# Kernel optimization log

Hardware: AMD Instinct MI355X
Metric: run time of the kernel (lower is better)

The kernel has to match this reference:

```python
import jax, jax.numpy as jnp
import numpy as np

B, IN_DIM, D, C = 4096, 1024, 128, 10000
H, HD = 4, 32  # heads, head_dim (D = H*HD)
EXP = 4        # ffn expansion
LN_EPS = 1e-5


def _ln(x, g, b):
    m = x.mean(-1, keepdims=True)
    v = ((x - m) ** 2).mean(-1, keepdims=True)
    return (x - m) / jnp.sqrt(v + LN_EPS) * g + b


def setup_inputs() -> dict:
    key = jax.random.key(0)
    ks = jax.random.split(key, 16)
    s = 0.02
    return {
        "x": jax.random.normal(ks[0], (B, IN_DIM), jnp.float32),
        # projector
        "W1": jax.random.normal(ks[1], (IN_DIM, 2 * D), jnp.float32) * s,
        "b1": jnp.zeros((2 * D,), jnp.float32),
        "W2": jax.random.normal(ks[2], (2 * D, D), jnp.float32) * s,
        "b2": jnp.zeros((D,), jnp.float32),
        # fractal block: MHA
        "in_w": jax.random.normal(ks[3], (D, 3 * D), jnp.float32) * s,
        "in_b": jnp.zeros((3 * D,), jnp.float32),
        "out_w": jax.random.normal(ks[4], (D, D), jnp.float32) * s,
        "out_b": jnp.zeros((D,), jnp.float32),
        # fractal block: FFN
        "fw1": jax.random.normal(ks[5], (D, EXP * D), jnp.float32) * s,
        "fb1": jnp.zeros((EXP * D,), jnp.float32),
        "fw2": jax.random.normal(ks[6], (EXP * D, D), jnp.float32) * s,
        "fb2": jnp.zeros((D,), jnp.float32),
        # layernorms
        "g1": jnp.ones((D,), jnp.float32), "bt1": jnp.zeros((D,), jnp.float32),
        "g2": jnp.ones((D,), jnp.float32), "bt2": jnp.zeros((D,), jnp.float32),
        # curvature, prototypes, euclidean head
        "log_c": jnp.array(0.0, jnp.float32),  # log(1.0)
        "prototypes": jax.random.normal(ks[7], (C, D), jnp.float32) * 0.1,
        "euc_w": jax.random.normal(ks[8], (D, C), jnp.float32) * s,
        "euc_b": jnp.zeros((C,), jnp.float32),
    }


def reference(x, W1, b1, W2, b2, in_w, in_b, out_w, out_b,
              fw1, fb1, fw2, fb2, g1, bt1, g2, bt2,
              log_c, prototypes, euc_w, euc_b):
    # ---- projector MLP (exact GELU, as torch default) ----
    t = jax.nn.gelu(x @ W1 + b1, approximate=False) @ W2 + b2  # (B, D)

    # ---- FractalBlock on seq_len=1 ----
    xs = t[:, None, :]  # (B, 1, D)
    qkv = xs @ in_w + in_b  # (B, 1, 3D)
    q, k, v = jnp.split(qkv, 3, axis=-1)
    q = q.reshape(B, 1, H, HD)
    k = k.reshape(B, 1, H, HD)
    v = v.reshape(B, 1, H, HD)
    scores = jnp.einsum("bqhd,bkhd->bhqk", q, k) / jnp.sqrt(jnp.float32(HD))
    w = jax.nn.softmax(scores, axis=-1)  # seq=1 -> all ones
    attn = jnp.einsum("bhqk,bkhd->bqhd", w, v).reshape(B, 1, D)
    attn = attn @ out_w + out_b
    xs = _ln(xs + attn, g1, bt1)
    ffn = jax.nn.gelu(xs @ fw1 + fb1, approximate=False) @ fw2 + fb2
    xs = _ln(xs + ffn, g2, bt2)
    t = xs[:, 0, :]  # (B, D) tangent

    # ---- curvature ----
    c = jnp.clip(jnp.exp(log_c), 1e-4, 10.0)
    c = jnp.maximum(jnp.abs(c), 1e-6)
    sqrt_c = jnp.sqrt(c)

    # ---- exp map to Poincare ball ----
    v_norm = jnp.maximum(jnp.linalg.norm(t, axis=-1, keepdims=True), 1e-10)
    emb = jnp.tanh(sqrt_c * v_norm / 2) * t / (sqrt_c * v_norm)
    e_norm = jnp.linalg.norm(emb, axis=-1, keepdims=True)
    max_norm = (1 - 1e-5) / sqrt_c
    emb = emb * jnp.minimum(max_norm / jnp.maximum(e_norm, 1e-6), 1.0)  # (B, D)

    # ---- project prototypes inside ball ----
    p_norm = jnp.linalg.norm(prototypes, axis=-1, keepdims=True)
    protos = prototypes * jnp.minimum(max_norm / jnp.maximum(p_norm, 1e-6), 1.0)  # (C, D)

    e2 = jnp.sum(emb * emb, axis=-1)      # (B,)
    p2 = jnp.sum(protos * protos, axis=-1)  # (C,)
    diff_sq = jnp.maximum(e2[:, None] + p2[None, :] - 2.0 * emb @ protos.T, 1e-10)  # (B, C)
    denom = (1 - c * jnp.minimum(e2, 1 - 1e-5))[:, None] * (1 - c * jnp.minimum(p2, 1 - 1e-5))[None, :]
    arg = 1 + 2 * diff_sq / jnp.maximum(denom, 1e-6)
    dists = 2 / sqrt_c * jnp.arccosh(jnp.maximum(arg, 1.0 + 1e-6))  # (B, C)

    hyp_logits = -dists
    euc_logits = t @ euc_w + euc_b
    return hyp_logits, euc_logits, emb
```

## Files before the change

### kernel.cpp

```cpp
#include <hip/hip_runtime.h>
#include <cmath>


using bf16x8 = __attribute__((ext_vector_type(8))) __bf16;
using f32x4  = __attribute__((ext_vector_type(4))) float;

#define DEVINL __device__ __forceinline__

DEVINL unsigned short f2b(float f) {
    unsigned int u = __builtin_bit_cast(unsigned int, f);
    u = (u + 0x7fffu + ((u >> 16) & 1u)) >> 16;
    return (unsigned short)u;
}

DEVINL float gelu_exact(float x) {
    return 0.5f * x * (1.0f + erff(x * 0.70710678118654752440f));
}

DEVINL float get_c(const float* logc) {
    float c = expf(logc[0]);
    c = fminf(fmaxf(c, 1e-4f), 10.0f);
    return fmaxf(fabsf(c), 1e-6f);
}

DEVINL void async16(const unsigned short* g, unsigned short* l) {
    __builtin_amdgcn_global_load_lds(
        (const __attribute__((address_space(1))) void*)g,
        (__attribute__((address_space(3))) void*)l, 16, 0, 0);
}


DEVINL void t_cvt(const float* __restrict__ src, unsigned short* __restrict__ dst,
                  int K, int N, int Npad, int ld, int off, int tblk, int tid,
                  float tile[32][33]) {
    int kbCount = K >> 5;
    int kb = (tblk % kbCount) * 32, nb = (tblk / kbCount) * 32;
    int tx = tid & 31, ty = tid >> 5;
    #pragma unroll
    for (int i = 0; i < 32; i += 8) {
        int k = kb + ty + i, n = nb + tx;
        tile[ty + i][tx] = (k < K && n < N) ? src[(size_t)k * ld + off + n] : 0.0f;
    }
    __syncthreads();
    #pragma unroll
    for (int i = 0; i < 32; i += 8) {
        int n = nb + ty + i, k = kb + tx;
        if (n < Npad && k < K) dst[(size_t)n * K + k] = f2b(tile[tx][ty + i]);
    }
}

#define PB0 4096
#define PB1 (PB0 + 256)
#define PB2 (PB1 + 64)
#define PB3 (PB2 + 64)
#define PB4 (PB3 + 1264)
#define PB5 (PB4 + 2528)

__global__ void k_prep(const float* __restrict__ x, const float* __restrict__ W1,
                       const float* __restrict__ fw1, const float* __restrict__ fw2,
                       const float* __restrict__ euc_w, const float* __restrict__ P,
                       const float* __restrict__ logc,
                       unsigned short* __restrict__ xbf, unsigned short* __restrict__ W1T,
                       unsigned short* __restrict__ FW1T, unsigned short* __restrict__ FW2T,
                       unsigned short* __restrict__ EUCWT, unsigned short* __restrict__ PROTB,
                       float* __restrict__ p2a, float* __restrict__ dpa) {
    __shared__ float tile[32][33];
    int b = blockIdx.x, tid = threadIdx.x;
    if (b < PB0) {
        int i = b * 256 + tid;
        float4 v = ((const float4*)x)[i];
        ushort4 o;
        o.x = f2b(v.x); o.y = f2b(v.y); o.z = f2b(v.z); o.w = f2b(v.w);
        ((ushort4*)xbf)[i] = o;
    } else if (b < PB1) {
        t_cvt(W1, W1T, 1024, 256, 256, 256, 0, b - PB0, tid, tile);
    } else if (b < PB2) {
        t_cvt(fw1, FW1T, 128, 512, 512, 512, 0, b - PB1, tid, tile);
    } else if (b < PB3) {
        t_cvt(fw2, FW2T, 512, 128, 128, 128, 0, b - PB2, tid, tile);
    } else if (b < PB4) {
        t_cvt(euc_w, EUCWT, 128, 10000, 10112, 10000, 0, b - PB3, tid, tile);
    } else {
        int lane = tid & 63;
        int row = (b - PB4) * 4 + (tid >> 6);
        size_t base = (size_t)row * 128;
        if (row < 10000) {
            float a = P[base + lane], bb = P[base + 64 + lane];
            float n2 = a * a + bb * bb;
            #pragma unroll
            for (int m = 32; m > 0; m >>= 1) n2 += __shfl_xor(n2, m, 64);
            float c = get_c(logc);
            float sq = sqrtf(c);
            float mx = (1.0f - 1e-5f) / sq;
            float pn = sqrtf(n2);
            float f = fminf(mx / fmaxf(pn, 1e-6f), 1.0f);
            a *= f; bb *= f;
            PROTB[base + lane] = f2b(a); PROTB[base + 64 + lane] = f2b(bb);
            if (lane == 0) {
                float p2 = n2 * f * f;
                p2a[row] = p2;
                dpa[row] = 1.0f - c * fminf(p2, 1.0f - 1e-5f);
            }
        } else if (row < 10112) {
            PROTB[base + lane] = 0; PROTB[base + 64 + lane] = 0;
            if (lane == 0) { p2a[row] = 0.0f; dpa[row] = 1.0f; }
        }
    }
}


__global__ void k_fold1(const float* __restrict__ in_w, const float* __restrict__ in_b,
                        const float* __restrict__ out_w, const float* __restrict__ out_b,
                        float* __restrict__ Wc, float* __restrict__ bc) {
    int n = threadIdx.x, k = blockIdx.x;
    if (k < 128) {
        float a = 0.f;
        for (int j = 0; j < 128; j++) a += in_w[k * 384 + 256 + j] * out_w[j * 128 + n];
        Wc[k * 128 + n] = a + ((k == n) ? 1.0f : 0.0f);
    } else {
        float a = 0.f;
        for (int j = 0; j < 128; j++) a += in_b[256 + j] * out_w[j * 128 + n];
        bc[n] = a + out_b[n];
    }
}

__global__ void k_fold2(const float* __restrict__ W2, const float* __restrict__ b2,
                        const float* __restrict__ Wc, const float* __restrict__ bc,
                        unsigned short* __restrict__ W2ppT, float* __restrict__ bpp) {
    int n = threadIdx.x, k = blockIdx.x;
    if (k < 256) {
        float a = 0.f;
        for (int j = 0; j < 128; j++) a += W2[k * 128 + j] * Wc[j * 128 + n];
        W2ppT[n * 256 + k] = f2b(a);
    } else {
        float a = 0.f;
        for (int j = 0; j < 128; j++) a += b2[j] * Wc[j * 128 + n];
        bpp[n] = a + bc[n];
    }
}

#define EP_GELU 0
#define EP_LN1 1
#define EP_LN2HYP 2

template <int EP, int BK>
__global__ __launch_bounds__(256) void k_gemm(
    const unsigned short* __restrict__ A, const unsigned short* __restrict__ Bm,
    const float* __restrict__ bias, int K, int Nstore,
    float* __restrict__ outF, unsigned short* __restrict__ outH,
    const float* __restrict__ g, const float* __restrict__ bt,
    const float* __restrict__ resF, const float* __restrict__ logc,
    float* __restrict__ embF, unsigned short* __restrict__ embH,
    float* __restrict__ e2a, float* __restrict__ dea) {
    __shared__ __align__(16) unsigned short As[128 * BK];
    __shared__ __align__(16) unsigned short Bs[128 * BK];
    const int tid = threadIdx.x, lane = tid & 63, wid = tid >> 6;
    const int row0 = blockIdx.x * 128, col0 = blockIdx.y * 128;
    const int q = lane >> 4, l16 = lane & 15;
    const int wm = (wid >> 1) * 64, wn = (wid & 1) * 64;
    constexpr int CPR = BK / 8;
    constexpr int ITER = 128 * CPR / 256;

    f32x4 acc[4][4];
    #pragma unroll
    for (int i = 0; i < 4; i++)
        #pragma unroll
        for (int j = 0; j < 4; j++) acc[i][j] = {0.f, 0.f, 0.f, 0.f};

    for (int k0 = 0; k0 < K; k0 += BK) {
        #pragma unroll
        for (int it = 0; it < ITER; ++it) {
            int idx = it * 256 + tid;
            int r = idx / CPR, ck = (idx % CPR) * 8;
            async16(&A[(size_t)(row0 + r) * K + k0 + ck], &As[idx * 8]);
        }
        #pragma unroll
        for (int it = 0; it < ITER; ++it) {
            int idx = it * 256 + tid;
            int r = idx / CPR, ck = (idx % CPR) * 8;
            async16(&Bm[(size_t)(col0 + r) * K + k0 + ck], &Bs[idx * 8]);
        }
        __syncthreads();
        #pragma unroll
        for (int kk = 0; kk < BK; kk += 32) {
            bf16x8 af[4], bfr[4];
            #pragma unroll
            for (int i = 0; i < 4; i++)
                af[i] = *(const bf16x8*)&As[(wm + i * 16 + l16) * BK + kk + q * 8];
            #pragma unroll
            for (int j = 0; j < 4; j++)
                bfr[j] = *(const bf16x8*)&Bs[(wn + j * 16 + l16) * BK + kk + q * 8];
            #pragma unroll
            for (int i = 0; i < 4; i++)
                #pragma unroll
                for (int j = 0; j < 4; j++)
                    acc[i][j] = __builtin_amdgcn_mfma_f32_16x16x32_bf16(
                        af[i], bfr[j], acc[i][j], 0, 0, 0);
        }
        __syncthreads();
    }

    if (EP == EP_GELU) {
        #pragma unroll
        for (int j = 0; j < 4; j++) {
            int col = col0 + wn + j * 16 + l16;
            float bb = bias[col];
            #pragma unroll
            for (int i = 0; i < 4; i++)
                #pragma unroll
                for (int rg = 0; rg < 4; rg++) {
                    int row = row0 + wm + i * 16 + q * 4 + rg;
                    outH[(size_t)row * Nstore + col] = f2b(gelu_exact(acc[i][j][rg] + bb));
                }
        }
        return;
    }

    #pragma unroll
    for (int j = 0; j < 4; j++) {
        int col = wn + j * 16 + l16;
        float bb = bias[col];
        #pragma unroll
        for (int i = 0; i < 4; i++)
            #pragma unroll
            for (int rg = 0; rg < 4; rg++) {
                int rl = wm + i * 16 + q * 4 + rg;
                float v = acc[i][j][rg] + bb;
                if (EP == EP_LN2HYP) v += resF[(size_t)(row0 + rl) * 128 + col];
                acc[i][j][rg] = v;
            }
    }
    float* sred = (float*)As;
    #pragma unroll
    for (int i = 0; i < 4; i++)
        #pragma unroll
        for (int rg = 0; rg < 4; rg++) {
            float s = 0.f, ss = 0.f;
            #pragma unroll
            for (int j = 0; j < 4; j++) { float v = acc[i][j][rg]; s += v; ss += v * v; }
            #pragma unroll
            for (int m = 1; m < 16; m <<= 1) {
                s += __shfl_xor(s, m, 64); ss += __shfl_xor(ss, m, 64);
            }
            if (l16 == 0) {
                int rl = wm + i * 16 + q * 4 + rg;
                sred[rl * 4 + (wid & 1) * 2] = s;
                sred[rl * 4 + (wid & 1) * 2 + 1] = ss;
            }
        }
    __syncthreads();

    float c = 0.f, sq = 0.f, mx = 0.f;
    if (EP == EP_LN2HYP) { c = get_c(logc); sq = sqrtf(c); mx = (1.0f - 1e-5f) / sq; }

    #pragma unroll
    for (int i = 0; i < 4; i++)
        #pragma unroll
        for (int rg = 0; rg < 4; rg++) {
            int rl = wm + i * 16 + q * 4 + rg;
            int row = row0 + rl;
            float sum = sred[rl * 4 + 0] + sred[rl * 4 + 2];
            float sqs = sred[rl * 4 + 1] + sred[rl * 4 + 3];
            float m = sum * (1.0f / 128.0f);
            float var = sqs * (1.0f / 128.0f) - m * m;
            float inv = rsqrtf(var + 1e-5f);
            #pragma unroll
            for (int j = 0; j < 4; j++) {
                int col = wn + j * 16 + l16;
                float y = (acc[i][j][rg] - m) * inv * g[col] + bt[col];
                acc[i][j][rg] = y;
                if (EP == EP_LN1) {
                    outF[(size_t)row * 128 + col] = y;
                    outH[(size_t)row * 128 + col] = f2b(y);
                } else {
                    outH[(size_t)row * 128 + col] = f2b(y);
                }
            }
        }

    if (EP == EP_LN2HYP) {
        float* sred2 = (float*)Bs;
        #pragma unroll
        for (int i = 0; i < 4; i++)
            #pragma unroll
            for (int rg = 0; rg < 4; rg++) {
                float s2 = 0.f;
                #pragma unroll
                for (int j = 0; j < 4; j++) { float y = acc[i][j][rg]; s2 += y * y; }
                #pragma unroll
                for (int m = 1; m < 16; m <<= 1) s2 += __shfl_xor(s2, m, 64);
                if (l16 == 0) {
                    int rl = wm + i * 16 + q * 4 + rg;
                    sred2[rl * 2 + (wid & 1)] = s2;
                }
            }
        __syncthreads();
        #pragma unroll
        for (int i = 0; i < 4; i++)
            #pragma unroll
            for (int rg = 0; rg < 4; rg++) {
                int rl = wm + i * 16 + q * 4 + rg;
                int row = row0 + rl;
                float vn2 = sred2[rl * 2] + sred2[rl * 2 + 1];
                float vn = fmaxf(sqrtf(vn2), 1e-10f);
                float sc = tanhf(0.5f * sq * vn) / (sq * vn);
                float en2 = sc * sc * vn2;
                float en = sqrtf(en2);
                float f = fminf(mx / fmaxf(en, 1e-6f), 1.0f);
                float scale = sc * f;
                float e2v = en2 * f * f;
                #pragma unroll
                for (int j = 0; j < 4; j++) {
                    int col = wn + j * 16 + l16;
                    float e = acc[i][j][rg] * scale;
                    embF[(size_t)row * 128 + col] = e;
                    embH[(size_t)row * 128 + col] = f2b(e);
                }
                if (l16 == 0 && (wid & 1) == 0) {
                    e2a[row] = e2v;
                    dea[row] = 1.0f - c * fminf(e2v, 1.0f - 1e-5f);
                }
            }
    }
}

__global__ __launch_bounds__(256) void k_heads(
    const unsigned short* __restrict__ embH, const unsigned short* __restrict__ tH,
    const unsigned short* __restrict__ protB, const unsigned short* __restrict__ eucWT,
    const float* __restrict__ e2a, const float* __restrict__ dea,
    const float* __restrict__ p2a, const float* __restrict__ dpa,
    const float* __restrict__ euc_b, const float* __restrict__ logc,
    float* __restrict__ outHyp, float* __restrict__ outEuc) {
    __shared__ __align__(16) unsigned short S[4096 * 8];
    const bool hyp = blockIdx.y < 79;
    const int cb = hyp ? blockIdx.y : blockIdx.y - 79;
    const unsigned short* Ap = hyp ? embH : tH;
    const unsigned short* Bp = hyp ? protB : eucWT;
    const int tid = threadIdx.x, lane = tid & 63, wid = tid >> 6;
    const int row0 = blockIdx.x * 128, col0 = cb * 128;
    const int q = lane >> 4, l16 = lane & 15;
    const int wm = (wid >> 1) * 64, wn = (wid & 1) * 64;

    #pragma unroll
    for (int it = 0; it < 16; ++it) {
        int idx = it * 256 + tid;
        if (idx < 2048) {
            int r = idx >> 4, ck = (idx & 15) * 8;
            async16(&Ap[(size_t)(row0 + r) * 128 + ck], &S[idx * 8]);
        } else {
            int idb = idx - 2048;
            int r = idb >> 4, ck = (idb & 15) * 8;
            async16(&Bp[(size_t)(col0 + r) * 128 + ck], &S[idx * 8]);
        }
    }
    __syncthreads();
    const unsigned short* As = S;
    const unsigned short* Bs = S + 2048 * 8;

    f32x4 acc[4][4];
    #pragma unroll
    for (int i = 0; i < 4; i++)
        #pragma unroll
        for (int j = 0; j < 4; j++) acc[i][j] = {0.f, 0.f, 0.f, 0.f};
    #pragma unroll
    for (int kk = 0; kk < 128; kk += 32) {
        bf16x8 af[4], bfr[4];
        #pragma unroll
        for (int i = 0; i < 4; i++)
            af[i] = *(const bf16x8*)&As[(wm + i * 16 + l16) * 128 + kk + q * 8];
        #pragma unroll
        for (int j = 0; j < 4; j++)
            bfr[j] = *(const bf16x8*)&Bs[(wn + j * 16 + l16) * 128 + kk + q * 8];
        #pragma unroll
        for (int i = 0; i < 4; i++)
            #pragma unroll
            for (int j = 0; j < 4; j++)
                acc[i][j] = __builtin_amdgcn_mfma_f32_16x16x32_bf16(
                    af[i], bfr[j], acc[i][j], 0, 0, 0);
    }

    if (hyp) {
        float c = get_c(logc);
        float invsq = 2.0f / sqrtf(c);
        #pragma unroll
        for (int j = 0; j < 4; j++) {
            int col = col0 + wn + j * 16 + l16;
            if (col < 10000) {
                float p2v = p2a[col], dpv = dpa[col];
                #pragma unroll
                for (int i = 0; i < 4; i++)
                    #pragma unroll
                    for (int rg = 0; rg < 4; rg++) {
                        int row = row0 + wm + i * 16 + q * 4 + rg;
                        float v = acc[i][j][rg];
                        float diff = fmaxf(e2a[row] + p2v - 2.0f * v, 1e-10f);
                        float den = fmaxf(dea[row] * dpv, 1e-6f);
                        float arg = fmaxf(1.0f + 2.0f * diff / den, 1.0f + 1e-6f);
                        float d = __logf(arg + sqrtf(arg * arg - 1.0f));
                        outHyp[(size_t)row * 10000 + col] = -invsq * d;
                    }
            }
        }
    } else {
        #pragma unroll
        for (int j = 0; j < 4; j++) {
            int col = col0 + wn + j * 16 + l16;
            if (col < 10000) {
                float bb = euc_b[col];
                #pragma unroll
                for (int i = 0; i < 4; i++)
                    #pragma unroll
                    for (int rg = 0; rg < 4; rg++) {
                        int row = row0 + wm + i * 16 + q * 4 + rg;
                        outEuc[(size_t)row * 10000 + col] = acc[i][j][rg] + bb;
                    }
            }
        }
    }
}


extern "C" void kernel_launch(void* const* d_in, const int* in_sizes, int n_in,
                              void* d_out, int out_size, void* d_ws, size_t ws_size,
                              hipStream_t stream) {
    const float* x      = (const float*)d_in[0];
    const float* W1     = (const float*)d_in[1];
    const float* b1     = (const float*)d_in[2];
    const float* W2     = (const float*)d_in[3];
    const float* b2     = (const float*)d_in[4];
    const float* in_w   = (const float*)d_in[5];
    const float* in_b   = (const float*)d_in[6];
    const float* out_w  = (const float*)d_in[7];
    const float* out_b  = (const float*)d_in[8];
    const float* fw1    = (const float*)d_in[9];
    const float* fb1    = (const float*)d_in[10];
    const float* fw2    = (const float*)d_in[11];
    const float* fb2    = (const float*)d_in[12];
    const float* g1     = (const float*)d_in[13];
    const float* bt1    = (const float*)d_in[14];
    const float* g2     = (const float*)d_in[15];
    const float* bt2    = (const float*)d_in[16];
    const float* logc   = (const float*)d_in[17];
    const float* protos = (const float*)d_in[18];
    const float* euc_w  = (const float*)d_in[19];
    const float* euc_b  = (const float*)d_in[20];

    float* out_hyp = (float*)d_out;
    float* out_euc = out_hyp + (size_t)4096 * 10000;
    float* out_emb = out_euc + (size_t)4096 * 10000;

    constexpr size_t O_XBF   = 0;
    constexpr size_t O_W1T   = O_XBF   + (size_t)4096 * 1024 * 2;
    constexpr size_t O_FW1T  = O_W1T   + (size_t)256 * 1024 * 2;
    constexpr size_t O_FW2T  = O_FW1T  + (size_t)512 * 128 * 2;
    constexpr size_t O_EUCWT = O_FW2T  + (size_t)128 * 512 * 2;
    constexpr size_t O_PROTB = O_EUCWT + (size_t)10112 * 128 * 2;
    constexpr size_t O_WC    = O_PROTB + (size_t)10112 * 128 * 2;
    constexpr size_t O_BC    = O_WC    + (size_t)128 * 128 * 4;
    constexpr size_t O_W2PP  = O_BC    + (size_t)128 * 4;
    constexpr size_t O_BPP   = O_W2PP  + (size_t)128 * 256 * 2;
    constexpr size_t O_HBF   = O_BPP   + (size_t)128 * 4;
    constexpr size_t O_XS1F  = O_HBF   + (size_t)4096 * 256 * 2;
    constexpr size_t O_XS1B  = O_XS1F  + (size_t)4096 * 128 * 4;
    constexpr size_t O_FHB   = O_XS1B  + (size_t)4096 * 128 * 2;
    constexpr size_t O_TFB   = O_FHB   + (size_t)4096 * 512 * 2;
    constexpr size_t O_EMBB  = O_TFB   + (size_t)4096 * 128 * 2;
    constexpr size_t O_E2    = O_EMBB  + (size_t)4096 * 128 * 2;
    constexpr size_t O_DE    = O_E2    + (size_t)4096 * 4;
    constexpr size_t O_P2    = O_DE    + (size_t)4096 * 4;
    constexpr size_t O_DP    = O_P2    + (size_t)10112 * 4;

    char* w = (char*)d_ws;
    auto US = [&](size_t o) { return (unsigned short*)(w + o); };
    auto FP = [&](size_t o) { return (float*)(w + o); };

    k_prep<<<PB5, 256, 0, stream>>>(x, W1, fw1, fw2, euc_w, protos, logc,
                                    US(O_XBF), US(O_W1T), US(O_FW1T), US(O_FW2T),
                                    US(O_EUCWT), US(O_PROTB), FP(O_P2), FP(O_DP));
    k_fold1<<<129, 128, 0, stream>>>(in_w, in_b, out_w, out_b, FP(O_WC), FP(O_BC));
    k_fold2<<<257, 128, 0, stream>>>(W2, b2, FP(O_WC), FP(O_BC), US(O_W2PP), FP(O_BPP));

    k_gemm<EP_GELU, 64><<<dim3(32, 2), 256, 0, stream>>>(
        US(O_XBF), US(O_W1T), b1, 1024, 256, nullptr, US(O_HBF),
        nullptr, nullptr, nullptr, nullptr, nullptr, nullptr, nullptr, nullptr);
    k_gemm<EP_LN1, 64><<<dim3(32, 1), 256, 0, stream>>>(
        US(O_HBF), US(O_W2PP), FP(O_BPP), 256, 128, FP(O_XS1F), US(O_XS1B),
        g1, bt1, nullptr, nullptr, nullptr, nullptr, nullptr, nullptr);
    k_gemm<EP_GELU, 128><<<dim3(32, 4), 256, 0, stream>>>(
        US(O_XS1B), US(O_FW1T), fb1, 128, 512, nullptr, US(O_FHB),
        nullptr, nullptr, nullptr, nullptr, nullptr, nullptr, nullptr, nullptr);
    k_gemm<EP_LN2HYP, 64><<<dim3(32, 1), 256, 0, stream>>>(
        US(O_FHB), US(O_FW2T), fb2, 512, 128, nullptr, US(O_TFB),
        g2, bt2, FP(O_XS1F), logc, out_emb, US(O_EMBB), FP(O_E2), FP(O_DE));
    k_heads<<<dim3(32, 158), 256, 0, stream>>>(
        US(O_EMBB), US(O_TFB), US(O_PROTB), US(O_EUCWT),
        FP(O_E2), FP(O_DE), FP(O_P2), FP(O_DP), euc_b, logc, out_hyp, out_euc);
}
```

Measured before the change: 591.3 us.

## Swizzle LDS tiles with XOR to avoid bank conflicts and fuse fold kernels

The change applies an XOR swizzle to the K-chunk index of both GEMM kernels. Each global-to-LDS async copy fetches a permuted source chunk, and the fragment reads use the matching XOR on the lane's row, which is meant to spread MFMA fragment loads across LDS banks. It also merges the two weight-folding kernels into one per-column kernel that keeps intermediate columns in shared memory, removing one launch and the Wc/bc workspace. The fused fold does serial per-thread dot products over strided global reads, and the bias is computed by a single thread per block.

```diff
diff --git a/kernel.cpp b/kernel.cpp
--- a/kernel.cpp
+++ b/kernel.cpp
@@ -108,34 +108,32 @@
     }
 }
 
-
-__global__ void k_fold1(const float* __restrict__ in_w, const float* __restrict__ in_b,
-                        const float* __restrict__ out_w, const float* __restrict__ out_b,
-                        float* __restrict__ Wc, float* __restrict__ bc) {
-    int n = threadIdx.x, k = blockIdx.x;
-    if (k < 128) {
-        float a = 0.f;
-        for (int j = 0; j < 128; j++) a += in_w[k * 384 + 256 + j] * out_w[j * 128 + n];
-        Wc[k * 128 + n] = a + ((k == n) ? 1.0f : 0.0f);
-    } else {
-        float a = 0.f;
-        for (int j = 0; j < 128; j++) a += in_b[256 + j] * out_w[j * 128 + n];
-        bc[n] = a + out_b[n];
-    }
-}
-
-__global__ void k_fold2(const float* __restrict__ W2, const float* __restrict__ b2,
-                        const float* __restrict__ Wc, const float* __restrict__ bc,
-                        unsigned short* __restrict__ W2ppT, float* __restrict__ bpp) {
-    int n = threadIdx.x, k = blockIdx.x;
-    if (k < 256) {
-        float a = 0.f;
-        for (int j = 0; j < 128; j++) a += W2[k * 128 + j] * Wc[j * 128 + n];
-        W2ppT[n * 256 + k] = f2b(a);
-    } else {
-        float a = 0.f;
-        for (int j = 0; j < 128; j++) a += b2[j] * Wc[j * 128 + n];
-        bpp[n] = a + bc[n];
+__global__ void k_fold(const float* __restrict__ in_w, const float* __restrict__ in_b,
+                       const float* __restrict__ out_w, const float* __restrict__ out_b,
+                       const float* __restrict__ W2, const float* __restrict__ b2,
+                       unsigned short* __restrict__ W2ppT, float* __restrict__ bpp) {
+    __shared__ float WoCol[128];
+    __shared__ float WcCol[128];
+    const int n = blockIdx.x, t = threadIdx.x;
+    WoCol[t] = out_w[t * 128 + n];
+    __syncthreads();
+    float a = (t == n) ? 1.0f : 0.0f;
+    for (int j = 0; j < 128; j++) a += in_w[t * 384 + 256 + j] * WoCol[j];
+    WcCol[t] = a;
+    __syncthreads();
+    #pragma unroll
+    for (int h = 0; h < 2; h++) {
+        int k = t + h * 128;
+        float s = 0.f;
+        for (int j = 0; j < 128; j++) s += W2[k * 128 + j] * WcCol[j];
+        W2ppT[n * 256 + k] = f2b(s);
+    }
+    if (t == 0) {
+        float s = 0.f;
+        for (int j = 0; j < 128; j++) s += b2[j] * WcCol[j];
+        float s2 = 0.f;
+        for (int j = 0; j < 128; j++) s2 += in_b[256 + j] * WoCol[j];
+        bpp[n] = s + s2 + out_b[n];
     }
 }
 
@@ -158,6 +156,7 @@
     const int row0 = blockIdx.x * 128, col0 = blockIdx.y * 128;
     const int q = lane >> 4, l16 = lane & 15;
     const int wm = (wid >> 1) * 64, wn = (wid & 1) * 64;
+    const int sw = (l16 & 7) * 8;
     constexpr int CPR = BK / 8;
     constexpr int ITER = 128 * CPR / 256;
 
@@ -172,13 +171,15 @@
         for (int it = 0; it < ITER; ++it) {
             int idx = it * 256 + tid;
             int r = idx / CPR, ck = (idx % CPR) * 8;
-            async16(&A[(size_t)(row0 + r) * K + k0 + ck], &As[idx * 8]);
+            int cks = ck ^ ((r & 7) * 8);
+            async16(&A[(size_t)(row0 + r) * K + k0 + cks], &As[idx * 8]);
         }
         #pragma unroll
         for (int it = 0; it < ITER; ++it) {
             int idx = it * 256 + tid;
             int r = idx / CPR, ck = (idx % CPR) * 8;
-            async16(&Bm[(size_t)(col0 + r) * K + k0 + ck], &Bs[idx * 8]);
+            int cks = ck ^ ((r & 7) * 8);
+            async16(&Bm[(size_t)(col0 + r) * K + k0 + cks], &Bs[idx * 8]);
         }
         __syncthreads();
         #pragma unroll
@@ -186,10 +187,10 @@
             bf16x8 af[4], bfr[4];
             #pragma unroll
             for (int i = 0; i < 4; i++)
-                af[i] = *(const bf16x8*)&As[(wm + i * 16 + l16) * BK + kk + q * 8];
+                af[i] = *(const bf16x8*)&As[(wm + i * 16 + l16) * BK + ((kk + q * 8) ^ sw)];
             #pragma unroll
             for (int j = 0; j < 4; j++)
-                bfr[j] = *(const bf16x8*)&Bs[(wn + j * 16 + l16) * BK + kk + q * 8];
+                bfr[j] = *(const bf16x8*)&Bs[(wn + j * 16 + l16) * BK + ((kk + q * 8) ^ sw)];
             #pragma unroll
             for (int i = 0; i < 4; i++)
                 #pragma unroll
@@ -340,17 +341,20 @@
     const int row0 = blockIdx.x * 128, col0 = cb * 128;
     const int q = lane >> 4, l16 = lane & 15;
     const int wm = (wid >> 1) * 64, wn = (wid & 1) * 64;
+    const int sw = (l16 & 7) * 8;
 
     #pragma unroll
     for (int it = 0; it < 16; ++it) {
         int idx = it * 256 + tid;
         if (idx < 2048) {
             int r = idx >> 4, ck = (idx & 15) * 8;
-            async16(&Ap[(size_t)(row0 + r) * 128 + ck], &S[idx * 8]);
+            int cks = ck ^ ((r & 7) * 8);
+            async16(&Ap[(size_t)(row0 + r) * 128 + cks], &S[idx * 8]);
         } else {
             int idb = idx - 2048;
             int r = idb >> 4, ck = (idb & 15) * 8;
-            async16(&Bp[(size_t)(col0 + r) * 128 + ck], &S[idx * 8]);
+            int cks = ck ^ ((r & 7) * 8);
+            async16(&Bp[(size_t)(col0 + r) * 128 + cks], &S[idx * 8]);
         }
     }
     __syncthreads();
@@ -367,10 +371,10 @@
         bf16x8 af[4], bfr[4];
         #pragma unroll
         for (int i = 0; i < 4; i++)
-            af[i] = *(const bf16x8*)&As[(wm + i * 16 + l16) * 128 + kk + q * 8];
+            af[i] = *(const bf16x8*)&As[(wm + i * 16 + l16) * 128 + ((kk + q * 8) ^ sw)];
         #pragma unroll
         for (int j = 0; j < 4; j++)
-            bfr[j] = *(const bf16x8*)&Bs[(wn + j * 16 + l16) * 128 + kk + q * 8];
+            bfr[j] = *(const bf16x8*)&Bs[(wn + j * 16 + l16) * 128 + ((kk + q * 8) ^ sw)];
         #pragma unroll
         for (int i = 0; i < 4; i++)
             #pragma unroll
@@ -455,9 +459,7 @@
     constexpr size_t O_FW2T  = O_FW1T  + (size_t)512 * 128 * 2;
     constexpr size_t O_EUCWT = O_FW2T  + (size_t)128 * 512 * 2;
     constexpr size_t O_PROTB = O_EUCWT + (size_t)10112 * 128 * 2;
-    constexpr size_t O_WC    = O_PROTB + (size_t)10112 * 128 * 2;
-    constexpr size_t O_BC    = O_WC    + (size_t)128 * 128 * 4;
-    constexpr size_t O_W2PP  = O_BC    + (size_t)128 * 4;
+    constexpr size_t O_W2PP  = O_PROTB + (size_t)10112 * 128 * 2;
     constexpr size_t O_BPP   = O_W2PP  + (size_t)128 * 256 * 2;
     constexpr size_t O_HBF   = O_BPP   + (size_t)128 * 4;
     constexpr size_t O_XS1F  = O_HBF   + (size_t)4096 * 256 * 2;
@@ -477,8 +479,8 @@
     k_prep<<<PB5, 256, 0, stream>>>(x, W1, fw1, fw2, euc_w, protos, logc,
                                     US(O_XBF), US(O_W1T), US(O_FW1T), US(O_FW2T),
                                     US(O_EUCWT), US(O_PROTB), FP(O_P2), FP(O_DP));
-    k_fold1<<<129, 128, 0, stream>>>(in_w, in_b, out_w, out_b, FP(O_WC), FP(O_BC));
-    k_fold2<<<257, 128, 0, stream>>>(W2, b2, FP(O_WC), FP(O_BC), US(O_W2PP), FP(O_BPP));
+    k_fold<<<128, 128, 0, stream>>>(in_w, in_b, out_w, out_b, W2, b2,
+                                    US(O_W2PP), FP(O_BPP));
 
     k_gemm<EP_GELU, 64><<<dim3(32, 2), 256, 0, stream>>>(
         US(O_XBF), US(O_W1T), b1, 1024, 256, nullptr, US(O_HBF),
```

Result: no change. 584.3 us (-1.2%).
